# Performance work log

Hardware: AMD Instinct MI355X
Metric: run time of the kernel (lower is better)

## Reference

```python
import jax, jax.numpy as jnp
import numpy as np

V_REST = 0.0
V_RESET = 0.0
V_TH = 1.27
TAU = 50.0
SPIKE_DURATION = 1
SCALE = 100.0  # SurrGradSpike.scale


@jax.custom_vjp
def spike(x):
    return (x > 0).astype(x.dtype)

def _spike_fwd(x):
    return (x > 0).astype(x.dtype), x

def _spike_bwd(x, g):
    # normalized negative part of fast sigmoid (Zenke & Ganguli 2018)
    return (g / (SCALE * jnp.abs(x) + 1.0) ** 2,)

spike.defvjp(_spike_fwd, _spike_bwd)


def _shift(a, k):
    # a[:, j] -> a[:, j + k], zero padded out of range
    if k == 0:
        return a
    if k > 0:
        return jnp.pad(a[:, k:], ((0, 0), (0, k)))
    return jnp.pad(a[:, :k], ((0, 0), (-k, 0)))


def _lif(ode, decay):
    ode2 = ode[..., 0]          # [B, T]
    B, T = ode2.shape
    ode_t = ode2.T              # [T, B] for scan

    def step(carry, inp):
        v, counter, z = carry   # z = remaining steps whose dv reads are zeroed
        t, x = inp
        v = v - decay * (v - V_REST)
        v = jnp.where(counter == 1, V_RESET, v)
        # dv[:, t] was zeroed by a spike within the previous 5 steps (torch in-place window)
        x_eff = jnp.where(z > 0, 0.0, x)
        v = v + x_eff
        v = jnp.where(counter > 1, V_TH, v)
        s = spike(v - V_TH)
        s_d = jax.lax.stop_gradient(s)
        counter = counter + (SPIKE_DURATION + 1) * s_d
        v = jnp.where(counter > 1, V_TH, v)
        # spike at t zeroes dv[:, t-1:t+6]; at t==0 the torch slice [-1:6] is empty
        z = jnp.where((s_d > 0) & (t >= 1), 5.0, jnp.maximum(z - 1.0, 0.0))
        counter = jnp.maximum(counter - 1.0, 0.0)
        return (v, counter, z), (v, s, s_d)

    v0 = jnp.full((B,), V_REST, dtype=ode2.dtype)
    c0 = jnp.zeros((B,), dtype=ode2.dtype)
    z0 = jnp.zeros((B,), dtype=ode2.dtype)
    ts = jnp.arange(T)
    _, (v_rec, s_rec, sd_rec) = jax.lax.scan(step, (v0, c0, z0), (ts, ode_t))
    v_rec = v_rec.T             # [B, T]
    s_rec = s_rec.T             # [B, T]

    sp = sd_rec.T > 0           # detached spike mask [B, T]
    sp = sp.at[:, 0].set(False)  # spike at t=0 zeroes nothing (empty slice in torch)
    # column j of dv is zeroed iff a spike occurred at t' in [j-5, j+1]
    zero_mask = jnp.zeros_like(sp)
    for k in range(-5, 2):
        zero_mask = zero_mask | _shift(sp, k)
    dv = jnp.where(zero_mask, 0.0, ode2)
    return v_rec, s_rec, dv


def setup_inputs() -> dict:
    key = jax.random.key(0)
    B, T = 2048, 4096
    ode = jax.random.normal(key, (B, T, 1), dtype=jnp.float32)
    decay = jnp.float32(1.0 / TAU)  # LIF.decay parameter (learn_tau=False)
    return {"ode": ode, "decay": decay}


def reference(ode, decay):
    return _lif(ode, decay)
```

## Files before the change

kernel.cpp:

```cpp
#include <hip/hip_runtime.h>

constexpr int   T   = 4096;
constexpr float VTH = 1.27f;
constexpr int   K   = 16;
constexpr int   L   = T / K;
constexpr int   LG  = L / 4;
constexpr int   WGG = 160;

__device__ __forceinline__ bool sstep(float x, float decay, float& v, unsigned& h, bool& gate) {
    float t1 = __fmul_rn(decay, v);
    float vd = __fsub_rn(v, t1);
    float xe = gate ? 0.0f : x;
    float vn = __fadd_rn(vd, xe);
    bool  s  = vn > VTH;
    v = s ? 0.0f : vn;
    bool g4 = (h & 15u) != 0u;
    h = (h << 1) | (s ? 1u : 0u);
    gate = s || g4;
    return s;
}

__device__ __forceinline__ bool ostep(float x, float decay, float& v, unsigned& h, bool& gate,
                                      float& vo, float& so, float& dvo, float xprev) {
    float t1 = __fmul_rn(decay, v);
    float vd = __fsub_rn(v, t1);
    float xe = gate ? 0.0f : x;
    float vn = __fadd_rn(vd, xe);
    bool  s  = vn > VTH;
    vo = s ? VTH  : vn;
    so = s ? 1.0f : 0.0f;
    v  = s ? 0.0f : vn;
    bool z6 = s || ((h & 63u) != 0u);
    dvo = z6 ? 0.0f : xprev;
    bool g4 = (h & 15u) != 0u;
    h = (h << 1) | (s ? 1u : 0u);
    gate = s || g4;
    return s;
}

__device__ __forceinline__ void ogroup(float4 X, float decay, float& v, unsigned& h, bool& gate,
                                       float& xprev, float4& vo, float4& so,
                                       float& close, float& px, float& py, float& pz) {
    ostep(X.x, decay, v, h, gate, vo.x, so.x, close, xprev); xprev = X.x;
    ostep(X.y, decay, v, h, gate, vo.y, so.y, px,    xprev); xprev = X.y;
    ostep(X.z, decay, v, h, gate, vo.z, so.z, py,    xprev); xprev = X.z;
    ostep(X.w, decay, v, h, gate, vo.w, so.w, pz,    xprev); xprev = X.w;
}

#define WVM(N) do { asm volatile("s_waitcnt vmcnt(" #N ")" ::: "memory"); \
                    __builtin_amdgcn_sched_barrier(0); } while (0)
#define WLG()  do { asm volatile("s_waitcnt lgkmcnt(0)" ::: "memory"); \
                    __builtin_amdgcn_sched_barrier(0); } while (0)

using GU32 = const __attribute__((address_space(1))) unsigned int;
using LU32 = __attribute__((address_space(3))) unsigned int;

__device__ __forceinline__ void stage8(const float* src0, float4* lbuf) {
    LU32* lp = (LU32*)lbuf;
#pragma unroll
    for (int j = 0; j < 8; ++j)
        __builtin_amdgcn_global_load_lds((GU32*)(src0 + (size_t)j * 8 * T),
                                         lp + j * 256, 16, 0, 0);
}

__global__ __launch_bounds__(64, 1)
void lif_spec(const float* __restrict__ ode, const float* __restrict__ decay_p,
              float* __restrict__ vout, float* __restrict__ sout, float* __restrict__ dvout,
              float2* __restrict__ Sst, float2* __restrict__ Est, int B) {
    __shared__ float4 xin[64 * 8];
    __shared__ float4 stgA[64 * 8];
    __shared__ float4 stgB[64 * 8];

    const int tid = threadIdx.x;
    const int gg  = blockIdx.x * 64;
    const int rb  = gg % B;
    const int k   = gg / B;
    const int b   = rb + tid;
    const float decay = decay_p[0];
    const int t7 = tid & 7, t3 = tid >> 3;
    const int sw = t7 ^ t3;

    const int g0f = k * LG;
    const int wgg = (k == 0) ? 0 : (g0f < WGG ? g0f : WGG);
    const int nw  = wgg >> 3;
    const int gstart = g0f - wgg;

    float v = 0.0f; unsigned h = 0u; bool gate = false;
    float xprev = 0.0f;

    float xla = (k < K - 1) ? ode[(size_t)b * T + (size_t)(k + 1) * L] : 0.0f;

#define STAGE(t) stage8(ode + ((size_t)(rb + t3) * T \
                               + (size_t)(gstart + 8 * (t)) * 4 + sw * 4), xin)
    float4 G0, G1, G2, G3, G4, G5, G6, G7;
#define RD8() do { G0 = xin[tid*8 + (0^t7)]; G1 = xin[tid*8 + (1^t7)]; \
                   G2 = xin[tid*8 + (2^t7)]; G3 = xin[tid*8 + (3^t7)]; \
                   G4 = xin[tid*8 + (4^t7)]; G5 = xin[tid*8 + (5^t7)]; \
                   G6 = xin[tid*8 + (6^t7)]; G7 = xin[tid*8 + (7^t7)]; } while (0)
#define WG4(G) { sstep(G.x, decay, v, h, gate); sstep(G.y, decay, v, h, gate); \
                 sstep(G.z, decay, v, h, gate); sstep(G.w, decay, v, h, gate); }

    STAGE(0);

    if (nw > 0) {
        const bool t0row = (gstart == 0);
        for (int t = 0; t < nw; ++t) {
            WVM(0);
            RD8();
            WLG();
            STAGE(t + 1);
            if (t == 0 && t0row) {
                sstep(G0.x, decay, v, h, gate); h = 0u; gate = false;
                sstep(G0.y, decay, v, h, gate);
                sstep(G0.z, decay, v, h, gate);
                sstep(G0.w, decay, v, h, gate);
            } else { WG4(G0) }
            WG4(G1) WG4(G2) WG4(G3) WG4(G4) WG4(G5) WG4(G6) WG4(G7)
        }
    }

    float4 VA0, VA1, VA2, VA3, VA4, VA5, VA6, VA7;
    float4 SA0, SA1, SA2, SA3, SA4, SA5, SA6, SA7;
    float4 DA0, DA1, DA2, DA3, DA4, DA5, DA6, DA7;
    float4 DB0, DB1, DB2, DB3, DB4, DB5, DB6, DB7;
    float dumm;

#define OGR(X, Vd, Sd, CloseL, Dd) { \
        ostep(X.x, decay, v, h, gate, Vd.x, Sd.x, CloseL, xprev); xprev = X.x; \
        ostep(X.y, decay, v, h, gate, Vd.y, Sd.y, Dd.x,   xprev); xprev = X.y; \
        ostep(X.z, decay, v, h, gate, Vd.z, Sd.z, Dd.y,   xprev); xprev = X.z; \
        ostep(X.w, decay, v, h, gate, Vd.w, Sd.w, Dd.z,   xprev); xprev = X.w; }

#define FLVS(poff) { \
        stgA[tid*8 + (0^t7)] = VA0; stgA[tid*8 + (1^t7)] = VA1; \
        stgA[tid*8 + (2^t7)] = VA2; stgA[tid*8 + (3^t7)] = VA3; \
        stgA[tid*8 + (4^t7)] = VA4; stgA[tid*8 + (5^t7)] = VA5; \
        stgA[tid*8 + (6^t7)] = VA6; stgA[tid*8 + (7^t7)] = VA7; \
        stgB[tid*8 + (0^t7)] = SA0; stgB[tid*8 + (1^t7)] = SA1; \
        stgB[tid*8 + (2^t7)] = SA2; stgB[tid*8 + (3^t7)] = SA3; \
        stgB[tid*8 + (4^t7)] = SA4; stgB[tid*8 + (5^t7)] = SA5; \
        stgB[tid*8 + (6^t7)] = SA6; stgB[tid*8 + (7^t7)] = SA7; \
        WLG(); \
        _Pragma("unroll") \
        for (int jj = 0; jj < 8; ++jj) { \
            int rr = jj * 8 + t3; \
            size_t off = (size_t)(rb + rr) * T + (size_t)k * L + (poff) * 32 + t7 * 4; \
            *(float4*)(vout + off) = stgA[rr * 8 + sw]; \
            *(float4*)(sout + off) = stgB[rr * 8 + sw]; \
        } \
        WLG(); }

#define FLDV(R0,R1,R2,R3,R4,R5,R6,R7, poff) { \
        stgA[tid*8 + (0^t7)] = R0; stgA[tid*8 + (1^t7)] = R1; \
        stgA[tid*8 + (2^t7)] = R2; stgA[tid*8 + (3^t7)] = R3; \
        stgA[tid*8 + (4^t7)] = R4; stgA[tid*8 + (5^t7)] = R5; \
        stgA[tid*8 + (6^t7)] = R6; stgA[tid*8 + (7^t7)] = R7; \
        WLG(); \
        _Pragma("unroll") \
        for (int jj = 0; jj < 8; ++jj) { \
            int rr = jj * 8 + t3; \
            size_t off = (size_t)(rb + rr) * T + (size_t)k * L + (poff) * 32 + t7 * 4; \
            *(float4*)(dvout + off) = stgA[rr * 8 + sw]; \
        } \
        WLG(); }

    {
        WVM(0);
        RD8();
        WLG();
        if (nw > 0) Sst[k * B + b] = make_float2(v, __uint_as_float(h & 127u));
        STAGE(nw + 1);
        if (k == 0) {
            bool s0 = ostep(G0.x, decay, v, h, gate, VA0.x, SA0.x, dumm, xprev); xprev = G0.x;
            h = 0u; gate = false;
            bool s1 = ostep(G0.y, decay, v, h, gate, VA0.y, SA0.y, DA0.x, xprev); xprev = G0.y;
            ostep(G0.z, decay, v, h, gate, VA0.z, SA0.z, DA0.y, xprev); xprev = G0.z;
            ostep(G0.w, decay, v, h, gate, VA0.w, SA0.w, DA0.z, xprev); xprev = G0.w;
            if (s0 && s1) VA0.z = VTH;
        } else {
            OGR(G0, VA0, SA0, dumm, DA0)
        }
        OGR(G1, VA1, SA1, DA0.w, DA1) OGR(G2, VA2, SA2, DA1.w, DA2)
        OGR(G3, VA3, SA3, DA2.w, DA3) OGR(G4, VA4, SA4, DA3.w, DA4)
        OGR(G5, VA5, SA5, DA4.w, DA5) OGR(G6, VA6, SA6, DA5.w, DA6)
        OGR(G7, VA7, SA7, DA6.w, DA7)
        FLVS(0)
    }

#define MPAIR(p, DP, DC, VMN) { \
        WVM(VMN); \
        RD8(); \
        WLG(); \
        if ((p) < 7) STAGE(nw + (p) + 1); \
        OGR(G0, VA0, SA0, (DP##7).w, DC##0) \
        FLDV(DP##0, DP##1, DP##2, DP##3, DP##4, DP##5, DP##6, DP##7, (p) - 1) \
        OGR(G1, VA1, SA1, (DC##0).w, DC##1) OGR(G2, VA2, SA2, (DC##1).w, DC##2) \
        OGR(G3, VA3, SA3, (DC##2).w, DC##3) OGR(G4, VA4, SA4, (DC##3).w, DC##4) \
        OGR(G5, VA5, SA5, (DC##4).w, DC##5) OGR(G6, VA6, SA6, (DC##5).w, DC##6) \
        OGR(G7, VA7, SA7, (DC##6).w, DC##7) \
        FLVS(p) }

    MPAIR(1, DA, DB, 16)
    MPAIR(2, DB, DA, 24)
    MPAIR(3, DA, DB, 24)
    MPAIR(4, DB, DA, 24)
    MPAIR(5, DA, DB, 24)
    MPAIR(6, DB, DA, 24)
    MPAIR(7, DA, DB, 24)
#undef MPAIR

    Est[k * B + b] = make_float2(v, __uint_as_float(h & 127u));

    if (k < K - 1) {
        float vo_, so_;
        ostep(xla, decay, v, h, gate, vo_, so_, DB7.w, xprev);
    } else {
        DB7.w = ((h & 63u) != 0u) ? 0.0f : xprev;
    }
    FLDV(DB0, DB1, DB2, DB3, DB4, DB5, DB6, DB7, 7)
#undef OGR
#undef FLVS
#undef FLDV
#undef RD8
#undef WG4
#undef STAGE
}

__global__ __launch_bounds__(64, 1)
void lif_fix(const float* __restrict__ ode, const float* __restrict__ decay_p,
             float* __restrict__ vout, float* __restrict__ sout, float* __restrict__ dvout,
             const float2* __restrict__ Sst, const float2* __restrict__ Est, int B) {
    const int b = blockIdx.x * 64 + threadIdx.x;
    const float decay = decay_p[0];

    float2 E  = Est[b];
    float2 S1 = Sst[B + b];
    float2 E1 = Est[B + b];
    for (int k = 1; k < K; ++k) {
        float2 S = S1, Ek = E1;
        if (k + 1 < K) { S1 = Sst[(k + 1) * B + b]; E1 = Est[(k + 1) * B + b]; }
        bool match = (S.x == E.x) && (__float_as_uint(S.y) == __float_as_uint(E.y));
        if (match) { E = Ek; continue; }

        const size_t bt = (size_t)b * T;
        const float4* __restrict__ x4 = (const float4*)(ode + bt);
        float4* __restrict__ v4 = (float4*)(vout + bt);
        float4* __restrict__ s4 = (float4*)(sout + bt);
        float4* __restrict__ d4 = (float4*)(dvout + bt);
        const int g0f = k * LG;

        float v = E.x; unsigned h = __float_as_uint(E.y);
        bool gate = (h & 31u) != 0u;
        float xprev = 0.0f;
        float4 pend;

        float4 Q0 = x4[g0f], Q1 = x4[g0f + 1], Q2 = x4[g0f + 2], Q3 = x4[g0f + 3];
        {
            float4 vo, so; float cl;
            ogroup(Q0, decay, v, h, gate, xprev, vo, so, cl, pend.x, pend.y, pend.z);
            v4[g0f] = vo; s4[g0f] = so;
            Q0 = x4[g0f + 4];
        }
#define FPROC(cc, Q) { float4 vo, so; float px, py, pz; \
            ogroup(Q, decay, v, h, gate, xprev, vo, so, pend.w, px, py, pz); \
            d4[g0f + (cc) - 1] = pend; \
            pend.x = px; pend.y = py; pend.z = pz; \
            v4[g0f + (cc)] = vo; s4[g0f + (cc)] = so; }
        FPROC(1, Q1) Q1 = x4[g0f + 5];
        FPROC(2, Q2) Q2 = x4[g0f + 6];
        FPROC(3, Q3) Q3 = x4[g0f + 7];
        for (int c0 = 4; c0 < LG; c0 += 4) {
            FPROC(c0,     Q0) Q0 = x4[g0f + (c0 + 4 < LG ? c0 + 4 : LG - 1)];
            FPROC(c0 + 1, Q1) Q1 = x4[g0f + (c0 + 5 < LG ? c0 + 5 : LG - 1)];
            FPROC(c0 + 2, Q2) Q2 = x4[g0f + (c0 + 6 < LG ? c0 + 6 : LG - 1)];
            FPROC(c0 + 3, Q3) Q3 = x4[g0f + (c0 + 7 < LG ? c0 + 7 : LG - 1)];
        }
#undef FPROC
        E = make_float2(v, __uint_as_float(h & 127u));
        if (k < K - 1) {
            float xla = ode[bt + (size_t)(k + 1) * L];
            float vo_, so_;
            ostep(xla, decay, v, h, gate, vo_, so_, pend.w, xprev);
        } else {
            pend.w = ((h & 63u) != 0u) ? 0.0f : xprev;
        }
        d4[g0f + LG - 1] = pend;
    }
}

extern "C" void kernel_launch(void* const* d_in, const int* in_sizes, int n_in,
                              void* d_out, int out_size, void* d_ws, size_t ws_size,
                              hipStream_t stream) {
    const float* ode   = (const float*)d_in[0];
    const float* decay = (const float*)d_in[1];
    float* out = (float*)d_out;

    const int BT = in_sizes[0];
    const int B  = BT / T;

    float* vout  = out;
    float* sout  = out + (size_t)BT;
    float* dvout = out + 2 * (size_t)BT;

    float2* Sst = (float2*)d_ws;
    float2* Est = Sst + (size_t)K * B;

    lif_spec<<<dim3((B * K) / 64), dim3(64), 0, stream>>>(ode, decay, vout, sout, dvout,
                                                          Sst, Est, B);
    lif_fix<<<dim3(B / 64), dim3(64), 0, stream>>>(ode, decay, vout, sout, dvout,
                                                   Sst, Est, B);
}
```

Baseline: 176.7 us.

## Double time-chunk count and triple-buffer LDS staging for deeper prefetch

Raises the number of time chunks from 16 to 32, so each chunk is half as long, more workgroups run in parallel, and the output loop shrinks from 8 to 4 groups. Replaces the single LDS input buffer with a three-slot ring, so the next two stages are in flight while the current one is read. The wait counts are relaxed so a wait no longer drains all outstanding loads. In exchange, each chunk's warm-up prefix becomes a larger share of its work, the fix-up kernel sees more chunk boundaries, and LDS use grows.

```diff
diff --git a/kernel.cpp b/kernel.cpp
--- a/kernel.cpp
+++ b/kernel.cpp
@@ -2,7 +2,7 @@
 
 constexpr int   T   = 4096;
 constexpr float VTH = 1.27f;
-constexpr int   K   = 16;
+constexpr int   K   = 32;
 constexpr int   L   = T / K;
 constexpr int   LG  = L / 4;
 constexpr int   WGG = 160;
@@ -67,7 +67,7 @@
 void lif_spec(const float* __restrict__ ode, const float* __restrict__ decay_p,
               float* __restrict__ vout, float* __restrict__ sout, float* __restrict__ dvout,
               float2* __restrict__ Sst, float2* __restrict__ Est, int B) {
-    __shared__ float4 xin[64 * 8];
+    __shared__ float4 xin[3 * 512];
     __shared__ float4 stgA[64 * 8];
     __shared__ float4 stgB[64 * 8];
 
@@ -90,25 +90,30 @@
 
     float xla = (k < K - 1) ? ode[(size_t)b * T + (size_t)(k + 1) * L] : 0.0f;
 
-#define STAGE(t) stage8(ode + ((size_t)(rb + t3) * T \
-                               + (size_t)(gstart + 8 * (t)) * 4 + sw * 4), xin)
+#define STAGE(t, sbase) stage8(ode + ((size_t)(rb + t3) * T \
+                               + (size_t)(gstart + 8 * (t)) * 4 + sw * 4), (sbase))
     float4 G0, G1, G2, G3, G4, G5, G6, G7;
-#define RD8() do { G0 = xin[tid*8 + (0^t7)]; G1 = xin[tid*8 + (1^t7)]; \
-                   G2 = xin[tid*8 + (2^t7)]; G3 = xin[tid*8 + (3^t7)]; \
-                   G4 = xin[tid*8 + (4^t7)]; G5 = xin[tid*8 + (5^t7)]; \
-                   G6 = xin[tid*8 + (6^t7)]; G7 = xin[tid*8 + (7^t7)]; } while (0)
+#define RD8(P) do { G0 = (P)[tid*8 + (0^t7)]; G1 = (P)[tid*8 + (1^t7)]; \
+                    G2 = (P)[tid*8 + (2^t7)]; G3 = (P)[tid*8 + (3^t7)]; \
+                    G4 = (P)[tid*8 + (4^t7)]; G5 = (P)[tid*8 + (5^t7)]; \
+                    G6 = (P)[tid*8 + (6^t7)]; G7 = (P)[tid*8 + (7^t7)]; } while (0)
 #define WG4(G) { sstep(G.x, decay, v, h, gate); sstep(G.y, decay, v, h, gate); \
                  sstep(G.z, decay, v, h, gate); sstep(G.w, decay, v, h, gate); }
 
-    STAGE(0);
+    STAGE(0, xin);
+    STAGE(1, xin + 512);
+    int sl = 0;
 
     if (nw > 0) {
         const bool t0row = (gstart == 0);
         for (int t = 0; t < nw; ++t) {
-            WVM(0);
-            RD8();
-            WLG();
-            STAGE(t + 1);
+            WVM(8);
+            RD8(xin + sl * 512);
+            {
+                int st = sl + 2; if (st >= 3) st -= 3;
+                STAGE(t + 2, xin + st * 512);
+            }
+            sl = (sl == 2) ? 0 : sl + 1;
             if (t == 0 && t0row) {
                 sstep(G0.x, decay, v, h, gate); h = 0u; gate = false;
                 sstep(G0.y, decay, v, h, gate);
@@ -165,11 +170,13 @@
         WLG(); }
 
     {
-        WVM(0);
-        RD8();
-        WLG();
+        WVM(8);
+        RD8(xin + sl * 512);
         if (nw > 0) Sst[k * B + b] = make_float2(v, __uint_as_float(h & 127u));
-        STAGE(nw + 1);
+        {   int st = sl + 2; if (st >= 3) st -= 3;
+            STAGE(nw + 2, xin + st * 512);
+        }
+        sl = (sl == 2) ? 0 : sl + 1;
         if (k == 0) {
             bool s0 = ostep(G0.x, decay, v, h, gate, VA0.x, SA0.x, dumm, xprev); xprev = G0.x;
             h = 0u; gate = false;
@@ -189,9 +196,12 @@
 
 #define MPAIR(p, DP, DC, VMN) { \
         WVM(VMN); \
-        RD8(); \
-        WLG(); \
-        if ((p) < 7) STAGE(nw + (p) + 1); \
+        RD8(xin + sl * 512); \
+        if ((p) <= 1 || k < K - 1) { \
+            int st = sl + 2; if (st >= 3) st -= 3; \
+            STAGE(nw + (p) + 2, xin + st * 512); \
+        } \
+        sl = (sl == 2) ? 0 : sl + 1; \
         OGR(G0, VA0, SA0, (DP##7).w, DC##0) \
         FLDV(DP##0, DP##1, DP##2, DP##3, DP##4, DP##5, DP##6, DP##7, (p) - 1) \
         OGR(G1, VA1, SA1, (DC##0).w, DC##1) OGR(G2, VA2, SA2, (DC##1).w, DC##2) \
@@ -200,13 +210,9 @@
         OGR(G7, VA7, SA7, (DC##6).w, DC##7) \
         FLVS(p) }
 
-    MPAIR(1, DA, DB, 16)
-    MPAIR(2, DB, DA, 24)
-    MPAIR(3, DA, DB, 24)
-    MPAIR(4, DB, DA, 24)
-    MPAIR(5, DA, DB, 24)
-    MPAIR(6, DB, DA, 24)
-    MPAIR(7, DA, DB, 24)
+    MPAIR(1, DA, DB, 24)
+    MPAIR(2, DB, DA, 40)
+    MPAIR(3, DA, DB, 40)
 #undef MPAIR
 
     Est[k * B + b] = make_float2(v, __uint_as_float(h & 127u));
@@ -217,7 +223,7 @@
     } else {
         DB7.w = ((h & 63u) != 0u) ? 0.0f : xprev;
     }
-    FLDV(DB0, DB1, DB2, DB3, DB4, DB5, DB6, DB7, 7)
+    FLDV(DB0, DB1, DB2, DB3, DB4, DB5, DB6, DB7, 3)
 #undef OGR
 #undef FLVS
 #undef FLDV
```

Result: faster. 170.2 us (-3.7%).
